# Performance work log

Hardware: AMD Instinct MI355X
Metric: run time of the kernel (lower is better)

Reference implementation:

```python
import jax, jax.numpy as jnp
import numpy as np

B, D, H, DR, DM = 16384, 384, 1024, 512, 1152
KP, KN = 3, 2
K = KP + KN
RG_C = 8.0

def setup_inputs() -> dict:
    key = jax.random.key(0)
    ks = jax.random.split(key, 24)
    def n(k, shape, scale=1.0):
        return jax.random.normal(k, shape, jnp.float32) * scale
    s = lambda fan: 1.0 / np.sqrt(fan).astype(np.float32)
    return dict(
        init_f=n(ks[0], (B, D)),
        head_embs=n(ks[1], (K, B, D)),
        pred_embs=n(ks[2], (K, B, D)),
        w_ap=n(ks[3], (D, 1), s(D)), b_ap=jnp.zeros((1,), jnp.float32),
        w_an=n(ks[4], (D, 1), s(D)), b_an=jnp.zeros((1,), jnp.float32),
        nt_w1=n(ks[5], (D, H), s(D)), nt_b1=jnp.zeros((H,), jnp.float32),
        nt_w2=n(ks[6], (H, D), s(H)), nt_b2=jnp.zeros((D,), jnp.float32),
        g1=jnp.ones((D,), jnp.float32),
        rg_wx=n(ks[7], (D, DR), s(D)), rg_bx=jnp.zeros((DR,), jnp.float32),
        rg_wy=n(ks[8], (D, DR), s(D)), rg_by=jnp.zeros((DR,), jnp.float32),
        rg_wr=n(ks[9], (DR, DR), s(DR)), rg_br=jnp.zeros((DR,), jnp.float32),
        rg_wi=n(ks[10], (DR, DR), s(DR)), rg_bi=jnp.zeros((DR,), jnp.float32),
        rg_lam=n(ks[11], (DR,), 0.5),
        rg_wo=n(ks[12], (DR, D), s(DR)), rg_bo=jnp.zeros((D,), jnp.float32),
        g2=jnp.ones((D,), jnp.float32),
        mlp_wg=n(ks[13], (D, DM), s(D)),
        mlp_wv=n(ks[14], (D, DM), s(D)),
        mlp_wo=n(ks[15], (DM, D), s(DM)),
        fa_wg=n(ks[16], (D, D), s(D)),
        fa_wv=n(ks[17], (D, D), s(D)),
        fa_wo=n(ks[18], (D, D), s(D)),
        fa_wl=n(ks[19], (D, 1), s(D)), fa_bl=jnp.zeros((1,), jnp.float32),
    )

def rmsnorm(x, g, eps=1e-6):
    return x * g * jax.lax.rsqrt(jnp.mean(x * x, axis=-1, keepdims=True) + eps)

def rg_lru(x, wr, br, wi, bi, lam):
    # x: [B, S, DR] -> gated linear recurrence over S (Griffin RG-LRU)
    a_base = -RG_C * jax.nn.softplus(lam)  # [DR]
    def step(h, xt):
        r = jax.nn.sigmoid(xt @ wr + br)
        i = jax.nn.sigmoid(xt @ wi + bi)
        log_a = a_base * r
        h = jnp.exp(log_a) * h + jnp.sqrt(1.0 - jnp.exp(2.0 * log_a)) * (i * xt)
        return h, h
    h0 = jnp.zeros((x.shape[0], x.shape[2]), x.dtype)
    _, ys = jax.lax.scan(step, h0, jnp.swapaxes(x, 0, 1))
    return jnp.swapaxes(ys, 0, 1)

def reference(init_f, head_embs, pred_embs, w_ap, b_ap, w_an, b_an,
              nt_w1, nt_b1, nt_w2, nt_b2, g1,
              rg_wx, rg_bx, rg_wy, rg_by, rg_wr, rg_br, rg_wi, rg_bi,
              rg_lam, rg_wo, rg_bo, g2, mlp_wg, mlp_wv, mlp_wo,
              fa_wg, fa_wv, fa_wo, fa_wl, fa_bl):
    # message passing: estimate_tail_emb(head, pred) = head + pred (TransE-style)
    msg = head_embs + pred_embs                       # [K, B, D]
    pos = jnp.transpose(msg[:KP], (1, 0, 2))          # [B, KP, D]
    neg = jnp.transpose(msg[KP:], (1, 0, 2))          # [B, KN, D]
    # signed residual for negated atomics: -m + MLP(m)
    neg = -neg + jax.nn.relu(neg @ nt_w1 + nt_b1) @ nt_w2 + nt_b2
    # grouped softmax attention over the positive / negative message lists
    aw_p = jax.nn.softmax(pos @ w_ap + b_ap, axis=1)  # [B, KP, 1]
    aw_n = jax.nn.softmax(neg @ w_an + b_an, axis=1)  # [B, KN, 1]
    x = jnp.concatenate([init_f[:, None, :], pos * aw_p, neg * aw_n], axis=1)  # [B, S=6, D]
    # Griffin block (depth=1): recurrent residual branch
    h = rmsnorm(x, g1)
    u = h @ rg_wx + rg_bx                             # [B, S, DR]
    y = rg_lru(u, rg_wr, rg_br, rg_wi, rg_bi, rg_lam)
    gate = jax.nn.gelu(h @ rg_wy + rg_by)
    x = x + (y * gate) @ rg_wo + rg_bo
    # gated-MLP residual branch
    h2 = rmsnorm(x, g2)
    x = x + (jax.nn.gelu(h2 @ mlp_wg) * (h2 @ mlp_wv)) @ mlp_wo
    # final attention aggregation: Gated_MLP_block -> Linear(D,1) -> softmax -> mean
    fa = (jax.nn.gelu(x @ fa_wg) * (x @ fa_wv)) @ fa_wo
    w = jax.nn.softmax(fa @ fa_wl + fa_bl, axis=1)    # [B, S, 1]
    return jnp.mean(x * w, axis=1)                    # [B, D], agg_func='mean'
```

## Files before the change

kernel.cpp:

```cpp
#include <hip/hip_runtime.h>
#include <hip/hip_bf16.h>

#define B_TOT 16384
#define DD    384
#define HH    1024
#define DRR   512
#define DMM   1152
#define SS    6
#define KPP   3
#define KNN   2

typedef unsigned short ushort_t;
typedef __bf16 bf16x8 __attribute__((ext_vector_type(8)));
typedef float  f32x4  __attribute__((ext_vector_type(4)));

__device__ __forceinline__ float fexp2(float x) { return __builtin_amdgcn_exp2f(x); }
__device__ __forceinline__ float frcp(float x)  { return __builtin_amdgcn_rcpf(x); }
__device__ __forceinline__ float sigmoid_f(float x) {
    return frcp(1.f + fexp2(-1.4426950408889634f * x));
}
__device__ __forceinline__ float gelu_f(float x) {
    float z = 0.7978845608028654f * x * (1.f + 0.044715f * x * x);
    return x * frcp(1.f + fexp2(-2.885390081777927f * z));
}
__device__ __forceinline__ float wave_red_sum(float v) {
    #pragma unroll
    for (int off = 32; off; off >>= 1) v += __shfl_xor(v, off);
    return v;
}
__device__ __forceinline__ ushort_t f2bf(float v) {
    __hip_bfloat16 h = __float2bfloat16(v);
    return *reinterpret_cast<ushort_t*>(&h);
}
__device__ __forceinline__ float bf2f(ushort_t u) {
    unsigned int x = ((unsigned int)u) << 16;
    return __uint_as_float(x);
}
__device__ __forceinline__ void g2l16(const ushort_t* g, ushort_t* l) {
    __builtin_amdgcn_global_load_lds(
        (const __attribute__((address_space(1))) void*)g,
        (__attribute__((address_space(3))) void*)l, 16, 0, 0);
}
__device__ __forceinline__ void swz_xy(int& bx, int& by) {
    const int nx = gridDim.x;
    const int nwg = nx * gridDim.y;
    const int h = by * nx + bx;
    const int q = nwg >> 3, r = nwg & 7;
    const int xcd = h & 7, lo = h >> 3;
    const int lin = (xcd < r) ? (xcd * (q + 1) + lo)
                              : (r * (q + 1) + (xcd - r) * q + lo);
    bx = lin % nx;
    by = lin / nx;
}

template<int EPI, bool ACCUM>
__global__ __launch_bounds__(256, 4)
void bgemm(const ushort_t* __restrict__ A, const ushort_t* __restrict__ WT,
           const float* __restrict__ bias, const ushort_t* __restrict__ X2,
           float* __restrict__ C, ushort_t* __restrict__ Ch, ushort_t* __restrict__ Ch2,
           int M, int N, int K)
{
    __shared__ ushort_t sm[16384];

    int bx = blockIdx.x, by = blockIdx.y;
    swz_xy(bx, by);
    const int tid = threadIdx.x;
    const int l = tid & 63, w = tid >> 6;
    const int wr = w >> 1, wc = w & 1;
    const int lr = l & 15, hi = l >> 4;
    const int row0 = by * 128, col0 = bx * 128;

    const int lrw = l >> 3;
    const int lch = (l & 7) ^ (lrw & 7);
    const ushort_t* As[4]; const ushort_t* Bs[4]; int lo_[4];
    #pragma unroll
    for (int i = 0; i < 4; ++i) {
        const int g = w * 4 + i;
        As[i] = A  + (size_t)(row0 + g*8 + lrw) * K + lch * 8;
        Bs[i] = WT + (size_t)(col0 + g*8 + lrw) * K + lch * 8;
        lo_[i] = g * 512;
    }
    const int ko[2] = {(hi*8) ^ ((lr&7)*8), (32 + hi*8) ^ ((lr&7)*8)};

    f32x4 acc[4][4] = {};
    const int NT = K >> 6;

    #pragma unroll
    for (int i = 0; i < 4; ++i) {
        g2l16(As[i], &sm[lo_[i]]);
        g2l16(Bs[i], &sm[8192 + lo_[i]]);
    }
    for (int t = 0; t < NT; ++t) {
        __syncthreads();
        #pragma unroll
        for (int ks = 0; ks < 2; ++ks) {
            bf16x8 af[4], bfr[4];
            #pragma unroll
            for (int m = 0; m < 4; ++m)
                af[m] = *(const bf16x8*)&sm[(wr*64 + m*16 + lr)*64 + ko[ks]];
            #pragma unroll
            for (int n = 0; n < 4; ++n)
                bfr[n] = *(const bf16x8*)&sm[8192 + (wc*64 + n*16 + lr)*64 + ko[ks]];
            #pragma unroll
            for (int m = 0; m < 4; ++m)
                #pragma unroll
                for (int n = 0; n < 4; ++n)
                    acc[m][n] = __builtin_amdgcn_mfma_f32_16x16x32_bf16(
                        af[m], bfr[n], acc[m][n], 0, 0, 0);
        }
        __syncthreads();
        if (t + 1 < NT) {
            #pragma unroll
            for (int i = 0; i < 4; ++i) {
                g2l16(As[i] + (size_t)(t+1)*64, &sm[lo_[i]]);
                g2l16(Bs[i] + (size_t)(t+1)*64, &sm[8192 + lo_[i]]);
            }
        }
    }

    const bool BF = (EPI == 7) || (Ch != nullptr);
    #pragma unroll
    for (int m = 0; m < 4; ++m) {
        #pragma unroll
        for (int n = 0; n < 4; ++n) {
            const int r0 = row0 + wr*64 + m*16 + hi*4;
            const int c  = col0 + wc*64 + n*16 + lr;
            const float bv = bias ? bias[c] : 0.f;
            const int rl0 = wr*64 + m*16 + hi*4;
            const int cl  = wc*64 + n*16 + lr;
            #pragma unroll
            for (int j = 0; j < 4; ++j) {
                const int r = r0 + j;
                float v = acc[m][n][j] + bv;
                if (EPI == 1) v = fmaxf(v, 0.f);
                if (EPI == 4) v = v - bf2f(X2[(size_t)r * N + c]);
                if (ACCUM)    v += C[(size_t)r * N + c];
                if (C) C[(size_t)r * N + c] = v;
                if (BF) {
                    float ov = (EPI == 7 && c >= 512) ? gelu_f(v) : v;
                    const int rl = rl0 + j;
                    sm[rl*128 + ((((cl>>3) ^ (rl & 7))) << 3) + (cl & 7)] = f2bf(ov);
                }
            }
        }
    }
    if (BF) {
        __syncthreads();
        const int er = tid >> 1, ec = (tid & 1) * 64;
        ushort_t* dst; int nn, dc0;
        if (EPI == 7) {
            nn = 512;
            if (col0 < 512) { dst = Ch;  dc0 = col0; }
            else            { dst = Ch2; dc0 = col0 - 512; }
        } else { dst = Ch; nn = N; dc0 = col0; }
        ushort_t* gp = dst + (size_t)(row0 + er) * nn + dc0 + ec;
        #pragma unroll
        for (int qq = 0; qq < 8; ++qq) {
            const int q = (ec >> 3) + qq;
            const uint4 vv = *(const uint4*)&sm[er*128 + ((q ^ (er & 7)) << 3)];
            *(uint4*)(gp + qq*8) = vv;
        }
    }
}

template<bool LOGITS>
__global__ __launch_bounds__(256, 4)
void dual_k(const ushort_t* __restrict__ A, const ushort_t* __restrict__ W1T,
            const ushort_t* __restrict__ W2T, ushort_t* __restrict__ Ch,
            float* __restrict__ LP, const float* __restrict__ wproj,
            int M, int N, int K)
{
    __shared__ ushort_t sm[16384];

    int bx = blockIdx.x, by = blockIdx.y;
    swz_xy(bx, by);
    const int tid = threadIdx.x;
    const int l = tid & 63, w = tid >> 6;
    const int wr = w >> 1, wc = w & 1;
    const int lr = l & 15, hi = l >> 4;
    const int row0 = by * 128, col0 = bx * 64;

    const int lrw = l >> 3;
    const int lch = (l & 7) ^ (lrw & 7);
    const ushort_t* As[4]; int loA[4];
    #pragma unroll
    for (int i = 0; i < 4; ++i) {
        const int g = w * 4 + i;
        As[i] = A + (size_t)(row0 + g*8 + lrw) * K + lch * 8;
        loA[i] = g * 512;
    }
    const ushort_t* Gs[2]; const ushort_t* Vs[2]; int loB[2];
    #pragma unroll
    for (int i = 0; i < 2; ++i) {
        const int g = w * 2 + i;
        Gs[i] = W1T + (size_t)(col0 + g*8 + lrw) * K + lch * 8;
        Vs[i] = W2T + (size_t)(col0 + g*8 + lrw) * K + lch * 8;
        loB[i] = g * 512;
    }
    const int ko[2] = {(hi*8) ^ ((lr&7)*8), (32 + hi*8) ^ ((lr&7)*8)};

    f32x4 ag[4][2] = {}, av[4][2] = {};
    const int NT = K >> 6;

    #pragma unroll
    for (int i = 0; i < 4; ++i) g2l16(As[i], &sm[loA[i]]);
    #pragma unroll
    for (int i = 0; i < 2; ++i) {
        g2l16(Gs[i], &sm[8192  + loB[i]]);
        g2l16(Vs[i], &sm[12288 + loB[i]]);
    }
    for (int t = 0; t < NT; ++t) {
        __syncthreads();
        #pragma unroll
        for (int ks = 0; ks < 2; ++ks) {
            bf16x8 af[4], bg[2], bv[2];
            #pragma unroll
            for (int m = 0; m < 4; ++m)
                af[m] = *(const bf16x8*)&sm[(wr*64 + m*16 + lr)*64 + ko[ks]];
            #pragma unroll
            for (int n = 0; n < 2; ++n) {
                bg[n] = *(const bf16x8*)&sm[8192  + (wc*32 + n*16 + lr)*64 + ko[ks]];
                bv[n] = *(const bf16x8*)&sm[12288 + (wc*32 + n*16 + lr)*64 + ko[ks]];
            }
            #pragma unroll
            for (int m = 0; m < 4; ++m)
                #pragma unroll
                for (int n = 0; n < 2; ++n) {
                    ag[m][n] = __builtin_amdgcn_mfma_f32_16x16x32_bf16(af[m], bg[n], ag[m][n], 0, 0, 0);
                    av[m][n] = __builtin_amdgcn_mfma_f32_16x16x32_bf16(af[m], bv[n], av[m][n], 0, 0, 0);
                }
        }
        __syncthreads();
        if (t + 1 < NT) {
            #pragma unroll
            for (int i = 0; i < 4; ++i)
                g2l16(As[i] + (size_t)(t+1)*64, &sm[loA[i]]);
            #pragma unroll
            for (int i = 0; i < 2; ++i) {
                g2l16(Gs[i] + (size_t)(t+1)*64, &sm[8192  + loB[i]]);
                g2l16(Vs[i] + (size_t)(t+1)*64, &sm[12288 + loB[i]]);
            }
        }
    }

    if (!LOGITS) {
        #pragma unroll
        for (int m = 0; m < 4; ++m)
            #pragma unroll
            for (int n = 0; n < 2; ++n) {
                const int cl = wc*32 + n*16 + lr;
                #pragma unroll
                for (int j = 0; j < 4; ++j) {
                    const int rl = wr*64 + m*16 + hi*4 + j;
                    sm[rl*64 + (((cl>>3) ^ (rl & 7)) << 3) + (cl & 7)] =
                        f2bf(gelu_f(ag[m][n][j]) * av[m][n][j]);
                }
            }
        __syncthreads();
        const int er = tid >> 1, ec = (tid & 1) * 32;
        ushort_t* gp = Ch + (size_t)(row0 + er) * N + col0 + ec;
        #pragma unroll
        for (int qq = 0; qq < 4; ++qq) {
            const int q = (ec >> 3) + qq;
            const uint4 vv = *(const uint4*)&sm[er*64 + ((q ^ (er & 7)) << 3)];
            *(uint4*)(gp + qq*8) = vv;
        }
    } else {
        float wp[2];
        #pragma unroll
        for (int n = 0; n < 2; ++n) wp[n] = wproj[col0 + wc*32 + n*16 + lr];
        float* red = (float*)sm;
        #pragma unroll
        for (int m = 0; m < 4; ++m) {
            #pragma unroll
            for (int j = 0; j < 4; ++j) {
                float s = 0.f;
                #pragma unroll
                for (int n = 0; n < 2; ++n)
                    s += gelu_f(ag[m][n][j]) * av[m][n][j] * wp[n];
                s += __shfl_xor(s, 1);
                s += __shfl_xor(s, 2);
                s += __shfl_xor(s, 4);
                s += __shfl_xor(s, 8);
                if (lr == 0) red[(wr*64 + m*16 + hi*4 + j) * 2 + wc] = s;
            }
        }
        __syncthreads();
        if (tid < 128)
            LP[(size_t)(row0 + tid) * 6 + bx] = red[tid*2] + red[tid*2 + 1];
    }
}

__global__ __launch_bounds__(256, 8)
void rec_k(ushort_t* __restrict__ u, const ushort_t* __restrict__ gate,
           const ushort_t* __restrict__ ri, const float* __restrict__ a2,
           int Bc)
{
    const int g = blockIdx.x * 256 + threadIdx.x;
    const int b = g >> 6, c8 = (g & 63) << 3;
    float a2v[8];
    *(float4*)&a2v[0] = *(const float4*)&a2[c8];
    *(float4*)&a2v[4] = *(const float4*)&a2[c8 + 4];
    float h[8] = {};
    for (int t = 0; t < SS; ++t) {
        const size_t row = (size_t)t * Bc + b;
        uint4 uw = *(const uint4*)&u[row * DRR + c8];
        uint4 rw = *(const uint4*)&ri[row * 1024 + c8];
        uint4 iw = *(const uint4*)&ri[row * 1024 + 512 + c8];
        uint4 gw = *(const uint4*)&gate[row * DRR + c8];
        const ushort_t* up = (const ushort_t*)&uw;
        const ushort_t* rp = (const ushort_t*)&rw;
        const ushort_t* ip = (const ushort_t*)&iw;
        const ushort_t* gp = (const ushort_t*)&gw;
        ushort_t o[8];
        #pragma unroll
        for (int q = 0; q < 8; ++q) {
            const float rv = sigmoid_f(bf2f(rp[q]));
            const float iv = sigmoid_f(bf2f(ip[q]));
            const float e  = fexp2(a2v[q] * rv);
            const float hv = e * h[q]
                           + sqrtf(fmaxf(0.f, 1.f - e * e)) * (iv * bf2f(up[q]));
            h[q] = hv;
            o[q] = f2bf(hv * bf2f(gp[q]));
        }
        *(uint4*)&u[row * DRR + c8] = *(const uint4*)o;
    }
}


struct TrArgs { const float* W[12]; };
__global__ void tr_all_k(TrArgs a, ushort_t* __restrict__ wt)
{
    constexpr int KT[12]  = {384,1024,384,384,512,512,512,384,384,1152,384,384};
    constexpr int NTb[12] = {1024,384,512,512,512,512,384,1152,1152,384,384,384};
    constexpr int EOFF[12]= {0,393216,786432,983040,1179648,1441792,1703936,
                             1900544,2342912,2785280,3227648,3375104};
    constexpr int TPRE[13]= {0,384,768,960,1152,1408,1664,1856,2288,2720,3152,3296,3440};
    const int tb = blockIdx.x;
    int s = 0;
    #pragma unroll
    for (int i = 0; i < 12; ++i) if (tb >= TPRE[i+1]) s = i + 1;
    const int rel = tb - TPRE[s];
    const int K = KT[s], N = NTb[s];
    const int ntn = N >> 5;
    const int k0 = (rel / ntn) * 32, n0 = (rel % ntn) * 32;

    __shared__ float ts[32][33];
    const int r = threadIdx.x >> 3, c4 = (threadIdx.x & 7) * 4;
    const float4 v = *(const float4*)&a.W[s][(size_t)(k0 + r) * N + n0 + c4];
    ts[r][c4+0] = v.x; ts[r][c4+1] = v.y; ts[r][c4+2] = v.z; ts[r][c4+3] = v.w;
    __syncthreads();
    ushort_t o4[4];
    #pragma unroll
    for (int q = 0; q < 4; ++q) o4[q] = f2bf(ts[c4 + q][r]);
    *(uint2*)&wt[EOFF[s] + (size_t)(n0 + r) * K + k0 + c4] = *(const uint2*)o4;
}

__global__ void prep_k(const float* __restrict__ rg_bx, const float* __restrict__ rg_by,
                       const float* __restrict__ rg_lam,
                       const float* __restrict__ rg_br, const float* __restrict__ rg_bi,
                       float* __restrict__ bias_xy, float* __restrict__ a2,
                       float* __restrict__ bias_ri)
{
    int i = blockIdx.x * 256 + threadIdx.x;
    if (i < 512) {
        bias_xy[i] = rg_bx[i];
        bias_ri[i] = rg_br[i];
        float lam = rg_lam[i];
        float sp = (lam > 20.f) ? lam : log1pf(expf(lam));
        a2[i] = -8.0f * sp * 1.4426950408889634f;
    } else if (i < 1024) {
        bias_xy[i] = rg_by[i - 512];
        bias_ri[i] = rg_bi[i - 512];
    }
}

__global__ void negm_k(const float* __restrict__ head, const float* __restrict__ pred,
                       ushort_t* __restrict__ negm_h, int b0, int Bc)
{
    int idx = blockIdx.x * 256 + threadIdx.x;
    int d = idx % DD, rr = idx / DD;
    int j = (rr >= Bc) ? 1 : 0;
    int b = rr - j * Bc;
    size_t off = ((size_t)(KPP + j) * B_TOT + (b0 + b)) * DD + d;
    negm_h[idx] = f2bf(head[off] + pred[off]);
}

__global__ void asmrms_k(const float* __restrict__ init_f,
                         const float* __restrict__ head, const float* __restrict__ pred,
                         const float* __restrict__ w_ap, const float* __restrict__ b_ap,
                         const float* __restrict__ w_an, const float* __restrict__ b_an,
                         const ushort_t* __restrict__ nf, const float* __restrict__ g1,
                         float* __restrict__ x, ushort_t* __restrict__ hb,
                         int b0, int Bc)
{
    const int lb = blockIdx.x, gb = b0 + lb, lane = threadIdx.x;
    float hp[3][6], nv[2][6], iv[6], wap[6], wan[6];
    #pragma unroll
    for (int q = 0; q < 6; ++q) {
        int d = lane + 64 * q;
        wap[q] = w_ap[d]; wan[q] = w_an[d];
        iv[q] = init_f[(size_t)gb * DD + d];
    }
    float lp[3], ln2[2];
    #pragma unroll
    for (int j = 0; j < 3; ++j) {
        float p = 0.f;
        #pragma unroll
        for (int q = 0; q < 6; ++q) {
            int d = lane + 64 * q;
            size_t off = ((size_t)j * B_TOT + gb) * DD + d;
            float v = head[off] + pred[off];
            hp[j][q] = v;
            p += v * wap[q];
        }
        lp[j] = wave_red_sum(p) + b_ap[0];
    }
    #pragma unroll
    for (int j = 0; j < 2; ++j) {
        float p = 0.f;
        #pragma unroll
        for (int q = 0; q < 6; ++q) {
            int d = lane + 64 * q;
            float v = bf2f(nf[((size_t)j * Bc + lb) * DD + d]);
            nv[j][q] = v;
            p += v * wan[q];
        }
        ln2[j] = wave_red_sum(p) + b_an[0];
    }
    float mp = fmaxf(lp[0], fmaxf(lp[1], lp[2]));
    float e0 = expf(lp[0]-mp), e1 = expf(lp[1]-mp), e2 = expf(lp[2]-mp);
    float sp = e0 + e1 + e2;
    float awp[3] = {e0/sp, e1/sp, e2/sp};
    float mn = fmaxf(ln2[0], ln2[1]);
    float f0 = expf(ln2[0]-mn), f1 = expf(ln2[1]-mn);
    float sn = f0 + f1;
    float awn[2] = {f0/sn, f1/sn};

    #pragma unroll
    for (int t = 0; t < SS; ++t) {
        float rowv[6], ss = 0.f;
        #pragma unroll
        for (int q = 0; q < 6; ++q) {
            float v;
            if (t == 0)      v = iv[q];
            else if (t <= 3) v = hp[t-1][q] * awp[t-1];
            else             v = nv[t-4][q] * awn[t-4];
            rowv[q] = v;
            ss += v * v;
        }
        ss = wave_red_sum(ss);
        float sc = rsqrtf(ss / (float)DD + 1e-6f);
        float* xr = x + (size_t)(t * Bc + lb) * DD;
        ushort_t* hr = hb + (size_t)(t * Bc + lb) * DD;
        #pragma unroll
        for (int q = 0; q < 6; ++q) {
            int d = lane + 64 * q;
            xr[d] = rowv[q];
            hr[d] = f2bf(rowv[q] * g1[d] * sc);
        }
    }
}

__global__ void rms_k(const float* __restrict__ x, const float* __restrict__ g,
                      ushort_t* __restrict__ h)
{
    int row  = blockIdx.x * 4 + (threadIdx.x >> 6);
    int lane = threadIdx.x & 63;
    const float* xr = x + (size_t)row * DD;
    float ss = 0.f;
    for (int d = lane; d < DD; d += 64) { float v = xr[d]; ss += v * v; }
    ss = wave_red_sum(ss);
    float sc = rsqrtf(ss / (float)DD + 1e-6f);
    ushort_t* hr = h + (size_t)row * DD;
    for (int d = lane; d < DD; d += 64) hr[d] = f2bf(xr[d] * g[d] * sc);
}

__global__ void wproj_k(const float* __restrict__ fa_wo, const float* __restrict__ fa_wl,
                        float* __restrict__ wproj)
{
    int d = threadIdx.x;
    float s = 0.f;
    for (int k = 0; k < DD; ++k) s += fa_wo[(size_t)d * DD + k] * fa_wl[k];
    wproj[d] = s;
}

__global__ void final_k(const float* __restrict__ x, const float* __restrict__ lp,
                        const float* __restrict__ fa_bl,
                        float* __restrict__ out, int b0, int Bc)
{
    const int lb = blockIdx.x, gb = b0 + lb, lane = threadIdx.x;
    float lg[SS];
    #pragma unroll
    for (int t = 0; t < SS; ++t) {
        const float* pp = lp + (size_t)(t * Bc + lb) * 6;
        lg[t] = pp[0] + pp[1] + pp[2] + pp[3] + pp[4] + pp[5] + fa_bl[0];
    }
    float m = lg[0];
    #pragma unroll
    for (int t = 1; t < SS; ++t) m = fmaxf(m, lg[t]);
    float e[SS], s = 0.f;
    #pragma unroll
    for (int t = 0; t < SS; ++t) { e[t] = expf(lg[t] - m); s += e[t]; }
    float inv = 1.0f / s;
    #pragma unroll
    for (int q = 0; q < 6; ++q) {
        int d = lane + 64 * q;
        float acc = 0.f;
        #pragma unroll
        for (int t = 0; t < SS; ++t)
            acc += x[(size_t)(t * Bc + lb) * DD + d] * (e[t] * inv);
        out[(size_t)gb * DD + d] = acc * (1.0f / 6.0f);
    }
}

extern "C" void kernel_launch(void* const* d_in, const int* in_sizes, int n_in,
                              void* d_out, int out_size, void* d_ws, size_t ws_size,
                              hipStream_t stream)
{
    (void)in_sizes; (void)n_in; (void)out_size;
    const float* init_f  = (const float*)d_in[0];
    const float* head    = (const float*)d_in[1];
    const float* pred    = (const float*)d_in[2];
    const float* w_ap    = (const float*)d_in[3];
    const float* b_ap    = (const float*)d_in[4];
    const float* w_an    = (const float*)d_in[5];
    const float* b_an    = (const float*)d_in[6];
    const float* nt_w1   = (const float*)d_in[7];
    const float* nt_b1   = (const float*)d_in[8];
    const float* nt_w2   = (const float*)d_in[9];
    const float* nt_b2   = (const float*)d_in[10];
    const float* g1      = (const float*)d_in[11];
    const float* rg_wx   = (const float*)d_in[12];
    const float* rg_bx   = (const float*)d_in[13];
    const float* rg_wy   = (const float*)d_in[14];
    const float* rg_by   = (const float*)d_in[15];
    const float* rg_wr   = (const float*)d_in[16];
    const float* rg_br   = (const float*)d_in[17];
    const float* rg_wi   = (const float*)d_in[18];
    const float* rg_bi   = (const float*)d_in[19];
    const float* rg_lam  = (const float*)d_in[20];
    const float* rg_wo   = (const float*)d_in[21];
    const float* rg_bo   = (const float*)d_in[22];
    const float* g2      = (const float*)d_in[23];
    const float* mlp_wg  = (const float*)d_in[24];
    const float* mlp_wv  = (const float*)d_in[25];
    const float* mlp_wo  = (const float*)d_in[26];
    const float* fa_wg   = (const float*)d_in[27];
    const float* fa_wv   = (const float*)d_in[28];
    const float* fa_wo   = (const float*)d_in[29];
    const float* fa_wl   = (const float*)d_in[30];
    const float* fa_bl   = (const float*)d_in[31];
    float* out = (float*)d_out;

    float* ws_f    = (float*)d_ws;
    float* wproj   = ws_f;
    float* bias_xy = ws_f + 512;
    float* a2      = ws_f + 1536;
    float* bias_ri = ws_f + 2048;
    ushort_t* wt   = (ushort_t*)(ws_f + 3072);

    ushort_t* ntw1T = wt + 0;
    ushort_t* ntw2T = wt + 393216;
    ushort_t* wxyT  = wt + 786432;
    ushort_t* wriT  = wt + 1179648;
    ushort_t* woT   = wt + 1703936;
    ushort_t* mwgT  = wt + 1900544;
    ushort_t* mwvT  = wt + 2342912;
    ushort_t* mwoT  = wt + 2785280;
    ushort_t* fwgT  = wt + 3227648;
    ushort_t* fwvT  = wt + 3375104;

    TrArgs ta;
    ta.W[0]=nt_w1; ta.W[1]=nt_w2; ta.W[2]=rg_wx; ta.W[3]=rg_wy;
    ta.W[4]=rg_wr; ta.W[5]=rg_wi; ta.W[6]=rg_wo; ta.W[7]=mlp_wg;
    ta.W[8]=mlp_wv; ta.W[9]=mlp_wo; ta.W[10]=fa_wg; ta.W[11]=fa_wv;
    tr_all_k<<<3440, 256, 0, stream>>>(ta, wt);
    prep_k<<<4, 256, 0, stream>>>(rg_bx, rg_by, rg_lam, rg_br, rg_bi,
                                  bias_xy, a2, bias_ri);
    wproj_k<<<1, DD, 0, stream>>>(fa_wo, fa_wl, wproj);

    const size_t fixed_f32 = 3072 + 1761280;
    const size_t per_b_f32 = 8448;
    int Bc = B_TOT;
    while (Bc > 128 && (fixed_f32 + per_b_f32 * (size_t)Bc) * 4 > ws_size) Bc >>= 1;

    float* arena = ws_f + fixed_f32;

    for (int b0 = 0; b0 < B_TOT; b0 += Bc) {
        const int M  = Bc * SS;
        const int M2 = Bc * KNN;
        float*    xbuf = arena;
        ushort_t* negm = (ushort_t*)(arena + (size_t)2304 * Bc);
        ushort_t* hid  = (ushort_t*)(arena + (size_t)2688 * Bc);
        ushort_t* nf   = (ushort_t*)(arena + (size_t)3712 * Bc);
        ushort_t* hb   = (ushort_t*)(arena + (size_t)4096 * Bc);
        ushort_t* uh   = (ushort_t*)(arena + (size_t)5376 * Bc);
        ushort_t* gth  = (ushort_t*)(arena + (size_t)6912 * Bc);
        ushort_t* ri   = (ushort_t*)(arena + (size_t)2304 * Bc);
        ushort_t* h2   = (ushort_t*)(arena + (size_t)2304 * Bc);
        ushort_t* Th   = (ushort_t*)(arena + (size_t)3456 * Bc);
        ushort_t* xh   = (ushort_t*)(arena + (size_t)6912 * Bc);
        float*    lpb  = arena + (size_t)2304 * Bc;

        negm_k<<<Bc * 3, 256, 0, stream>>>(head, pred, negm, b0, Bc);
        bgemm<1, false><<<dim3(HH/128, M2/128), 256, 0, stream>>>(
            negm, ntw1T, nt_b1, nullptr, nullptr, hid, nullptr, M2, HH, DD);
        bgemm<4, false><<<dim3(DD/128, M2/128), 256, 0, stream>>>(
            hid, ntw2T, nt_b2, negm, nullptr, nf, nullptr, M2, DD, HH);
        asmrms_k<<<Bc, 64, 0, stream>>>(init_f, head, pred, w_ap, b_ap, w_an, b_an,
                                        nf, g1, xbuf, hb, b0, Bc);

        bgemm<7, false><<<dim3(1024/128, M/128), 256, 0, stream>>>(
            hb, wxyT, bias_xy, nullptr, nullptr, uh, gth, M, 1024, DD);
        bgemm<0, false><<<dim3(1024/128, M/128), 256, 0, stream>>>(
            uh, wriT, bias_ri, nullptr, nullptr, ri, nullptr, M, 1024, DRR);
        rec_k<<<Bc / 4, 256, 0, stream>>>(uh, gth, ri, a2, Bc);
        bgemm<0, true><<<dim3(DD/128, M/128), 256, 0, stream>>>(
            uh, woT, rg_bo, nullptr, xbuf, nullptr, nullptr, M, DD, DRR);

        rms_k<<<M / 4, 256, 0, stream>>>(xbuf, g2, h2);
        dual_k<false><<<dim3(DMM/64, M/128), 256, 0, stream>>>(
            h2, mwgT, mwvT, Th, nullptr, nullptr, M, DMM, DD);
        bgemm<0, true><<<dim3(DD/128, M/128), 256, 0, stream>>>(
            Th, mwoT, nullptr, nullptr, xbuf, xh, nullptr, M, DD, DMM);

        dual_k<true><<<dim3(DD/64, M/128), 256, 0, stream>>>(
            xh, fwgT, fwvT, nullptr, lpb, wproj, M, DD, DD);
        final_k<<<Bc, 64, 0, stream>>>(xbuf, lpb, fa_bl, out, b0, Bc);
    }
}
```

Baseline: 1.468 ms.

## Load dual-GEMM weight fragments directly into registers instead of staging through LDS

```diff
diff --git a/kernel.cpp b/kernel.cpp
--- a/kernel.cpp
+++ b/kernel.cpp
@@ -164,13 +164,13 @@
 }
 
 template<bool LOGITS>
-__global__ __launch_bounds__(256, 4)
+__global__ __launch_bounds__(256, 3)
 void dual_k(const ushort_t* __restrict__ A, const ushort_t* __restrict__ W1T,
             const ushort_t* __restrict__ W2T, ushort_t* __restrict__ Ch,
             float* __restrict__ LP, const float* __restrict__ wproj,
             int M, int N, int K)
 {
-    __shared__ ushort_t sm[16384];
+    __shared__ ushort_t sm[8192];
 
     int bx = blockIdx.x, by = blockIdx.y;
     swz_xy(bx, by);
@@ -189,45 +189,46 @@
         As[i] = A + (size_t)(row0 + g*8 + lrw) * K + lch * 8;
         loA[i] = g * 512;
     }
-    const ushort_t* Gs[2]; const ushort_t* Vs[2]; int loB[2];
-    #pragma unroll
-    for (int i = 0; i < 2; ++i) {
-        const int g = w * 2 + i;
-        Gs[i] = W1T + (size_t)(col0 + g*8 + lrw) * K + lch * 8;
-        Vs[i] = W2T + (size_t)(col0 + g*8 + lrw) * K + lch * 8;
-        loB[i] = g * 512;
-    }
     const int ko[2] = {(hi*8) ^ ((lr&7)*8), (32 + hi*8) ^ ((lr&7)*8)};
+
+    const ushort_t* Gp[2]; const ushort_t* Vp[2];
+    #pragma unroll
+    for (int n = 0; n < 2; ++n) {
+        const int c = col0 + wc*32 + n*16 + lr;
+        Gp[n] = W1T + (size_t)c * K + hi*8;
+        Vp[n] = W2T + (size_t)c * K + hi*8;
+    }
 
     f32x4 ag[4][2] = {}, av[4][2] = {};
     const int NT = K >> 6;
 
     #pragma unroll
     for (int i = 0; i < 4; ++i) g2l16(As[i], &sm[loA[i]]);
-    #pragma unroll
-    for (int i = 0; i < 2; ++i) {
-        g2l16(Gs[i], &sm[8192  + loB[i]]);
-        g2l16(Vs[i], &sm[12288 + loB[i]]);
-    }
+    uint4 rg[2][2], rv[2][2];
+    #pragma unroll
+    for (int ks = 0; ks < 2; ++ks)
+        #pragma unroll
+        for (int n = 0; n < 2; ++n) {
+            rg[ks][n] = *(const uint4*)(Gp[n] + ks*32);
+            rv[ks][n] = *(const uint4*)(Vp[n] + ks*32);
+        }
+
     for (int t = 0; t < NT; ++t) {
         __syncthreads();
         #pragma unroll
         for (int ks = 0; ks < 2; ++ks) {
-            bf16x8 af[4], bg[2], bv[2];
+            bf16x8 af[4];
             #pragma unroll
             for (int m = 0; m < 4; ++m)
                 af[m] = *(const bf16x8*)&sm[(wr*64 + m*16 + lr)*64 + ko[ks]];
-            #pragma unroll
-            for (int n = 0; n < 2; ++n) {
-                bg[n] = *(const bf16x8*)&sm[8192  + (wc*32 + n*16 + lr)*64 + ko[ks]];
-                bv[n] = *(const bf16x8*)&sm[12288 + (wc*32 + n*16 + lr)*64 + ko[ks]];
-            }
             #pragma unroll
             for (int m = 0; m < 4; ++m)
                 #pragma unroll
                 for (int n = 0; n < 2; ++n) {
-                    ag[m][n] = __builtin_amdgcn_mfma_f32_16x16x32_bf16(af[m], bg[n], ag[m][n], 0, 0, 0);
-                    av[m][n] = __builtin_amdgcn_mfma_f32_16x16x32_bf16(af[m], bv[n], av[m][n], 0, 0, 0);
+                    ag[m][n] = __builtin_amdgcn_mfma_f32_16x16x32_bf16(
+                        af[m], *(const bf16x8*)&rg[ks][n], ag[m][n], 0, 0, 0);
+                    av[m][n] = __builtin_amdgcn_mfma_f32_16x16x32_bf16(
+                        af[m], *(const bf16x8*)&rv[ks][n], av[m][n], 0, 0, 0);
                 }
         }
         __syncthreads();
@@ -236,10 +237,12 @@
             for (int i = 0; i < 4; ++i)
                 g2l16(As[i] + (size_t)(t+1)*64, &sm[loA[i]]);
             #pragma unroll
-            for (int i = 0; i < 2; ++i) {
-                g2l16(Gs[i] + (size_t)(t+1)*64, &sm[8192  + loB[i]]);
-                g2l16(Vs[i] + (size_t)(t+1)*64, &sm[12288 + loB[i]]);
-            }
+            for (int ks = 0; ks < 2; ++ks)
+                #pragma unroll
+                for (int n = 0; n < 2; ++n) {
+                    rg[ks][n] = *(const uint4*)(Gp[n] + (size_t)(t+1)*64 + ks*32);
+                    rv[ks][n] = *(const uint4*)(Vp[n] + (size_t)(t+1)*64 + ks*32);
+                }
         }
     }
 
```

Result: slower. 1.720 ms (+17.2%).
